# Performance work log

Hardware: AMD Instinct MI355X
Metric: run time of the kernel (lower is better)

The kernel has to match this reference:

```python
import jax, jax.numpy as jnp
import numpy as np
import math

D_MODEL = 1024
NUM_HEADS = 16
D_K = D_MODEL // NUM_HEADS
MAX_LEN = 2048
BATCH = 2
SEQ = 2048


def setup_inputs() -> dict:
    key = jax.random.key(0)
    ks = jax.random.split(key, 12)
    w_scale = 0.02  # realistic init scale for linear weights
    inp = {
        "q": jax.random.normal(ks[0], (BATCH, SEQ, D_MODEL), jnp.float32),
        "k": jax.random.normal(ks[1], (BATCH, SEQ, D_MODEL), jnp.float32),
        "v": jax.random.normal(ks[2], (BATCH, SEQ, D_MODEL), jnp.float32),
        # learned params
        "rel_emb": jax.random.normal(ks[3], (2 * MAX_LEN, D_K), jnp.float32),
        "wq": jax.random.normal(ks[4], (D_MODEL, D_MODEL), jnp.float32) * w_scale,
        "bq": jnp.zeros((D_MODEL,), jnp.float32),
        "wk": jax.random.normal(ks[5], (D_MODEL, D_MODEL), jnp.float32) * w_scale,
        "bk": jnp.zeros((D_MODEL,), jnp.float32),
        "wv": jax.random.normal(ks[6], (D_MODEL, D_MODEL), jnp.float32) * w_scale,
        "bv": jnp.zeros((D_MODEL,), jnp.float32),
        "wo": jax.random.normal(ks[7], (D_MODEL, D_MODEL), jnp.float32) * w_scale,
        "bo": jnp.zeros((D_MODEL,), jnp.float32),
    }
    return inp


def reference(q, k, v, rel_emb, wq, bq, wk, bk, wv, bv, wo, bo):
    B, L, D = q.shape
    H, dk = NUM_HEADS, D // NUM_HEADS

    def split_heads(x):  # [B, L, D] -> [B, H, L, dk]
        return x.reshape(B, L, H, dk).transpose(0, 2, 1, 3)

    qh = split_heads(q @ wq.T + bq)
    kh = split_heads(k @ wk.T + bk)
    vh = split_heads(v @ wv.T + bv)

    # relative positions: rel_pos[i, j] = (j - i) + MAX_LEN, in [0, 2*MAX_LEN)
    r = jnp.arange(L)
    rel_pos = r[None, :] - r[:, None] + MAX_LEN  # [L, L] int32

    content_score = jnp.einsum("bhid,bhjd->bhij", qh, kh)
    # pos_score[b,h,i,j] = q[b,h,i,:] . rel_emb[rel_pos[i,j], :]
    rel = rel_emb[rel_pos]  # [L, L, dk]
    pos_score = jnp.einsum("bhid,ijd->bhij", qh, rel)

    scores = (content_score + pos_score) / math.sqrt(dk)
    attn = jax.nn.softmax(scores, axis=-1)
    out = jnp.einsum("bhij,bhjd->bhid", attn, vh)  # [B, H, L, dk]
    out = out.transpose(0, 2, 1, 3).reshape(B, L, D)
    return out @ wo.T + bo
```

## Files before the change

### kernel.cpp

```cpp
#include <hip/hip_runtime.h>
#include <hip/hip_fp16.h>


typedef _Float16 f16;
typedef _Float16 f16x4 __attribute__((ext_vector_type(4)));
typedef _Float16 f16x8 __attribute__((ext_vector_type(8)));
typedef float    f32x4 __attribute__((ext_vector_type(4)));

#define NBATCH 2
#define NHEADS 16
#define DKDIM  64
#define SEQL   2048
#define DMODEL 1024
#define NTOK   4096
#define MAXLEN 2048

__global__ void cvt_f32_f16(const float* __restrict__ src, f16* __restrict__ dst, int n4) {
    int i = blockIdx.x * blockDim.x + threadIdx.x;
    if (i < n4) {
        float4 v = ((const float4*)src)[i];
        f16x4 h = { (f16)v.x, (f16)v.y, (f16)v.z, (f16)v.w };
        ((f16x4*)dst)[i] = h;
    }
}

__global__ __launch_bounds__(256) void qkv_proj(
    const float* __restrict__ qg, const float* __restrict__ kg, const float* __restrict__ vg,
    const float* __restrict__ wq, const float* __restrict__ wk, const float* __restrict__ wv,
    const float* __restrict__ bq, const float* __restrict__ bk, const float* __restrict__ bv,
    f16* __restrict__ qh, f16* __restrict__ kh, f16* __restrict__ vt)
{
    const int which = blockIdx.z;
    const float* X    = which == 0 ? qg : (which == 1 ? kg : vg);
    const float* W    = which == 0 ? wq : (which == 1 ? wk : wv);
    const float* bias = which == 0 ? bq : (which == 1 ? bk : bv);

    __shared__ f16 As[128][40];
    __shared__ f16 Bs[128][40];

    const int tid = threadIdx.x;
    const int lane = tid & 63;
    const int w = tid >> 6;
    const int wr = w >> 1, wc = w & 1;
    const int row0 = blockIdx.y * 128;
    const int col0 = blockIdx.x * 128;

    f32x4 acc[4][4] = {};

    for (int kk = 0; kk < DMODEL; kk += 32) {
        #pragma unroll
        for (int rep = 0; rep < 4; ++rep) {
            int idx = rep * 256 + tid;
            int r = idx >> 3, seg = idx & 7;
            float4 va = *(const float4*)&X[(size_t)(row0 + r) * DMODEL + kk + seg * 4];
            f16x4 ha = { (f16)va.x, (f16)va.y, (f16)va.z, (f16)va.w };
            *(f16x4*)&As[r][seg * 4] = ha;
            float4 vb = *(const float4*)&W[(size_t)(col0 + r) * DMODEL + kk + seg * 4];
            f16x4 hb = { (f16)vb.x, (f16)vb.y, (f16)vb.z, (f16)vb.w };
            *(f16x4*)&Bs[r][seg * 4] = hb;
        }
        __syncthreads();

        f16x8 a[4], b[4];
        #pragma unroll
        for (int mi = 0; mi < 4; ++mi)
            a[mi] = *(const f16x8*)&As[wr * 64 + mi * 16 + (lane & 15)][(lane >> 4) * 8];
        #pragma unroll
        for (int ni = 0; ni < 4; ++ni)
            b[ni] = *(const f16x8*)&Bs[wc * 64 + ni * 16 + (lane & 15)][(lane >> 4) * 8];
        #pragma unroll
        for (int mi = 0; mi < 4; ++mi)
            #pragma unroll
            for (int ni = 0; ni < 4; ++ni)
                acc[mi][ni] = __builtin_amdgcn_mfma_f32_16x16x32_f16(a[mi], b[ni], acc[mi][ni], 0, 0, 0);
        __syncthreads();
    }

    #pragma unroll
    for (int mi = 0; mi < 4; ++mi) {
        #pragma unroll
        for (int ni = 0; ni < 4; ++ni) {
            int col = col0 + wc * 64 + ni * 16 + (lane & 15);
            int h = col >> 6, d = col & 63;
            float bc = bias[col];
            #pragma unroll
            for (int r = 0; r < 4; ++r) {
                int row = row0 + wr * 64 + mi * 16 + (lane >> 4) * 4 + r;
                int b_ = row >> 11, l = row & 2047;
                float val = acc[mi][ni][r] + bc;
                if (which == 0)
                    qh[((size_t)((b_ * 16 + h) * 2048 + l)) * 64 + d] = (f16)val;
                else if (which == 1)
                    kh[((size_t)((b_ * 16 + h) * 2048 + l)) * 64 + d] = (f16)val;
                else
                    vt[((size_t)((b_ * 16 + h) * 64 + d)) * 2048 + l] = (f16)val;
            }
        }
    }
}

__global__ __launch_bounds__(256) void flash_attn(
    const f16* __restrict__ qh, const f16* __restrict__ kh, const f16* __restrict__ vt,
    const f16* __restrict__ rel, f16* __restrict__ att)
{
    const int tid = threadIdx.x, lane = tid & 63, w = tid >> 6;
    const int bh = blockIdx.y;
    const int b = bh >> 4, h = bh & 15;
    const int i0 = blockIdx.x * 64;

    __shared__ f16 Ks[64][72];
    __shared__ f16 Vs[64][72];
    __shared__ f16 Rb[128][72];
    __shared__ f16 Qr[64][128];
    __shared__ f16 Ps[4][16][72];

    const size_t base_kq = (size_t)bh * SEQL * DKDIM;

    #pragma unroll
    for (int rep = 0; rep < 2; ++rep) {
        int idx = rep * 256 + tid;
        int r = idx >> 3, c8 = idx & 7;
        *(int4*)&Qr[r][c8 * 8] = *(const int4*)&qh[base_kq + (size_t)(i0 + r) * 64 + c8 * 8];
    }
    __syncthreads();
    f16x8 aq[2];
    aq[0] = *(const f16x8*)&Qr[w * 16 + (lane & 15)][(lane >> 4) * 8];
    aq[1] = *(const f16x8*)&Qr[w * 16 + (lane & 15)][32 + (lane >> 4) * 8];
    __syncthreads();

    float mrun[4], lrun[4];
    f32x4 oacc[4] = {};
    #pragma unroll
    for (int r = 0; r < 4; ++r) { mrun[r] = -1e30f; lrun[r] = 0.f; }

    for (int j0 = 0; j0 < SEQL; j0 += 64) {
        #pragma unroll
        for (int rep = 0; rep < 2; ++rep) {
            int idx = rep * 256 + tid;
            int r = idx >> 3, c8 = idx & 7;
            *(int4*)&Ks[r][c8 * 8] = *(const int4*)&kh[base_kq + (size_t)(j0 + r) * 64 + c8 * 8];
            *(int4*)&Vs[r][c8 * 8] = *(const int4*)&vt[base_kq + (size_t)r * 2048 + j0 + c8 * 8];
        }
        const int p0 = j0 - i0 - 63 + MAXLEN;
        #pragma unroll
        for (int rep = 0; rep < 4; ++rep) {
            int idx = rep * 256 + tid;
            int r = idx >> 3, c8 = idx & 7;
            int p = p0 + r; if (p > 4095) p = 4095;
            *(int4*)&Rb[r][c8 * 8] = *(const int4*)&rel[(size_t)p * 64 + c8 * 8];
        }
        __syncthreads();

        f32x4 sacc[4] = {};
        #pragma unroll
        for (int nf = 0; nf < 4; ++nf)
            #pragma unroll
            for (int ks = 0; ks < 2; ++ks) {
                f16x8 bk = *(const f16x8*)&Ks[nf * 16 + (lane & 15)][ks * 32 + (lane >> 4) * 8];
                sacc[nf] = __builtin_amdgcn_mfma_f32_16x16x32_f16(aq[ks], bk, sacc[nf], 0, 0, 0);
            }
        f32x4 qracc[8] = {};
        #pragma unroll
        for (int pf = 0; pf < 8; ++pf)
            #pragma unroll
            for (int ks = 0; ks < 2; ++ks) {
                f16x8 br = *(const f16x8*)&Rb[pf * 16 + (lane & 15)][ks * 32 + (lane >> 4) * 8];
                qracc[pf] = __builtin_amdgcn_mfma_f32_16x16x32_f16(aq[ks], br, qracc[pf], 0, 0, 0);
            }
        #pragma unroll
        for (int pf = 0; pf < 8; ++pf)
            #pragma unroll
            for (int r = 0; r < 4; ++r)
                Qr[w * 16 + (lane >> 4) * 4 + r][pf * 16 + (lane & 15)] = (f16)qracc[pf][r];
        __syncthreads();

        float p_[4][4];
        #pragma unroll
        for (int nf = 0; nf < 4; ++nf)
            #pragma unroll
            for (int r = 0; r < 4; ++r) {
                int gi = w * 16 + (lane >> 4) * 4 + r;
                int jl = nf * 16 + (lane & 15);
                p_[nf][r] = (sacc[nf][r] + (float)Qr[gi][jl - gi + 63]) * 0.125f;
            }
        float scale[4];
        #pragma unroll
        for (int r = 0; r < 4; ++r) {
            float mx = fmaxf(fmaxf(p_[0][r], p_[1][r]), fmaxf(p_[2][r], p_[3][r]));
            #pragma unroll
            for (int m = 8; m >= 1; m >>= 1) mx = fmaxf(mx, __shfl_xor(mx, m, 64));
            float mnew = fmaxf(mrun[r], mx);
            scale[r] = __expf(mrun[r] - mnew);
            float sm = 0.f;
            #pragma unroll
            for (int nf = 0; nf < 4; ++nf) { p_[nf][r] = __expf(p_[nf][r] - mnew); sm += p_[nf][r]; }
            #pragma unroll
            for (int m = 8; m >= 1; m >>= 1) sm += __shfl_xor(sm, m, 64);
            lrun[r] = lrun[r] * scale[r] + sm;
            mrun[r] = mnew;
        }
        #pragma unroll
        for (int df = 0; df < 4; ++df)
            #pragma unroll
            for (int r = 0; r < 4; ++r) oacc[df][r] *= scale[r];

        #pragma unroll
        for (int nf = 0; nf < 4; ++nf)
            #pragma unroll
            for (int r = 0; r < 4; ++r)
                Ps[w][(lane >> 4) * 4 + r][nf * 16 + (lane & 15)] = (f16)p_[nf][r];
        __syncthreads();
        f16x8 pa[2];
        pa[0] = *(const f16x8*)&Ps[w][lane & 15][(lane >> 4) * 8];
        pa[1] = *(const f16x8*)&Ps[w][lane & 15][32 + (lane >> 4) * 8];
        #pragma unroll
        for (int df = 0; df < 4; ++df)
            #pragma unroll
            for (int ks = 0; ks < 2; ++ks) {
                f16x8 bv = *(const f16x8*)&Vs[df * 16 + (lane & 15)][ks * 32 + (lane >> 4) * 8];
                oacc[df] = __builtin_amdgcn_mfma_f32_16x16x32_f16(pa[ks], bv, oacc[df], 0, 0, 0);
            }
        __syncthreads();
    }

    #pragma unroll
    for (int df = 0; df < 4; ++df) {
        int d = df * 16 + (lane & 15);
        #pragma unroll
        for (int r = 0; r < 4; ++r) {
            int i = i0 + w * 16 + (lane >> 4) * 4 + r;
            float val = oacc[df][r] / lrun[r];
            att[((size_t)(b * 2048 + i)) * DMODEL + h * 64 + d] = (f16)val;
        }
    }
}

__global__ __launch_bounds__(256) void out_proj(
    const f16* __restrict__ att, const f16* __restrict__ wo16, const float* __restrict__ bo,
    float* __restrict__ out)
{
    __shared__ f16 As[128][40];
    __shared__ f16 Bs[128][40];
    const int tid = threadIdx.x, lane = tid & 63, w = tid >> 6;
    const int wr = w >> 1, wc = w & 1;
    const int row0 = blockIdx.y * 128, col0 = blockIdx.x * 128;

    f32x4 acc[4][4] = {};

    for (int kk = 0; kk < DMODEL; kk += 32) {
        #pragma unroll
        for (int rep = 0; rep < 2; ++rep) {
            int idx = rep * 256 + tid;
            int r = idx >> 2, c8 = idx & 3;
            *(int4*)&As[r][c8 * 8] = *(const int4*)&att[(size_t)(row0 + r) * DMODEL + kk + c8 * 8];
            *(int4*)&Bs[r][c8 * 8] = *(const int4*)&wo16[(size_t)(col0 + r) * DMODEL + kk + c8 * 8];
        }
        __syncthreads();

        f16x8 a[4], b[4];
        #pragma unroll
        for (int mi = 0; mi < 4; ++mi)
            a[mi] = *(const f16x8*)&As[wr * 64 + mi * 16 + (lane & 15)][(lane >> 4) * 8];
        #pragma unroll
        for (int ni = 0; ni < 4; ++ni)
            b[ni] = *(const f16x8*)&Bs[wc * 64 + ni * 16 + (lane & 15)][(lane >> 4) * 8];
        #pragma unroll
        for (int mi = 0; mi < 4; ++mi)
            #pragma unroll
            for (int ni = 0; ni < 4; ++ni)
                acc[mi][ni] = __builtin_amdgcn_mfma_f32_16x16x32_f16(a[mi], b[ni], acc[mi][ni], 0, 0, 0);
        __syncthreads();
    }

    #pragma unroll
    for (int mi = 0; mi < 4; ++mi)
        #pragma unroll
        for (int ni = 0; ni < 4; ++ni) {
            int col = col0 + wc * 64 + ni * 16 + (lane & 15);
            float bc = bo[col];
            #pragma unroll
            for (int r = 0; r < 4; ++r) {
                int row = row0 + wr * 64 + mi * 16 + (lane >> 4) * 4 + r;
                out[(size_t)row * DMODEL + col] = acc[mi][ni][r] + bc;
            }
        }
}

extern "C" void kernel_launch(void* const* d_in, const int* in_sizes, int n_in,
                              void* d_out, int out_size, void* d_ws, size_t ws_size,
                              hipStream_t stream) {
    const float* q   = (const float*)d_in[0];
    const float* k   = (const float*)d_in[1];
    const float* v   = (const float*)d_in[2];
    const float* rel = (const float*)d_in[3];
    const float* wq  = (const float*)d_in[4];
    const float* bq  = (const float*)d_in[5];
    const float* wk  = (const float*)d_in[6];
    const float* bk  = (const float*)d_in[7];
    const float* wv  = (const float*)d_in[8];
    const float* bv  = (const float*)d_in[9];
    const float* wo  = (const float*)d_in[10];
    const float* bo  = (const float*)d_in[11];
    float* out = (float*)d_out;

    f16* ws    = (f16*)d_ws;
    f16* wo16  = ws;
    f16* rel16 = wo16 + (size_t)DMODEL * DMODEL;
    f16* qh16  = rel16 + (size_t)2 * MAXLEN * DKDIM;
    f16* kh16  = qh16 + (size_t)NTOK * DMODEL;
    f16* vt16  = kh16 + (size_t)NTOK * DMODEL;
    f16* att16 = vt16 + (size_t)NTOK * DMODEL;

    cvt_f32_f16<<<dim3(1024), 256, 0, stream>>>(wo, wo16, DMODEL * DMODEL / 4);
    cvt_f32_f16<<<dim3(256),  256, 0, stream>>>(rel, rel16, 2 * MAXLEN * DKDIM / 4);
    qkv_proj<<<dim3(8, 32, 3), 256, 0, stream>>>(q, k, v, wq, wk, wv, bq, bk, bv,
                                                 qh16, kh16, vt16);
    flash_attn<<<dim3(32, 32), 256, 0, stream>>>(qh16, kh16, vt16, rel16, att16);
    out_proj<<<dim3(8, 32), 256, 0, stream>>>(att16, wo16, bo, out);
}
```

Baseline: 438.7 us.

## Ring-buffer rel embeddings, per-wave pos band, deeper GEMM K tiles

After: 394.4 us. 1.11x faster.

```diff
diff --git a/kernel.cpp b/kernel.cpp
--- a/kernel.cpp
+++ b/kernel.cpp
@@ -35,8 +35,8 @@
     const float* W    = which == 0 ? wq : (which == 1 ? wk : wv);
     const float* bias = which == 0 ? bq : (which == 1 ? bk : bv);
 
-    __shared__ f16 As[128][40];
-    __shared__ f16 Bs[128][40];
+    __shared__ f16 As[128][72];
+    __shared__ f16 Bs[128][72];
 
     const int tid = threadIdx.x;
     const int lane = tid & 63;
@@ -47,11 +47,11 @@
 
     f32x4 acc[4][4] = {};
 
-    for (int kk = 0; kk < DMODEL; kk += 32) {
-        #pragma unroll
-        for (int rep = 0; rep < 4; ++rep) {
+    for (int kk = 0; kk < DMODEL; kk += 64) {
+        #pragma unroll
+        for (int rep = 0; rep < 8; ++rep) {
             int idx = rep * 256 + tid;
-            int r = idx >> 3, seg = idx & 7;
+            int r = idx >> 4, seg = idx & 15;
             float4 va = *(const float4*)&X[(size_t)(row0 + r) * DMODEL + kk + seg * 4];
             f16x4 ha = { (f16)va.x, (f16)va.y, (f16)va.z, (f16)va.w };
             *(f16x4*)&As[r][seg * 4] = ha;
@@ -61,18 +61,26 @@
         }
         __syncthreads();
 
-        f16x8 a[4], b[4];
+        f16x8 a[4][2], b[4][2];
         #pragma unroll
         for (int mi = 0; mi < 4; ++mi)
-            a[mi] = *(const f16x8*)&As[wr * 64 + mi * 16 + (lane & 15)][(lane >> 4) * 8];
+            #pragma unroll
+            for (int ks = 0; ks < 2; ++ks)
+                a[mi][ks] = *(const f16x8*)&As[wr * 64 + mi * 16 + (lane & 15)][ks * 32 + (lane >> 4) * 8];
         #pragma unroll
         for (int ni = 0; ni < 4; ++ni)
-            b[ni] = *(const f16x8*)&Bs[wc * 64 + ni * 16 + (lane & 15)][(lane >> 4) * 8];
+            #pragma unroll
+            for (int ks = 0; ks < 2; ++ks)
+                b[ni][ks] = *(const f16x8*)&Bs[wc * 64 + ni * 16 + (lane & 15)][ks * 32 + (lane >> 4) * 8];
+        __builtin_amdgcn_s_setprio(1);
         #pragma unroll
         for (int mi = 0; mi < 4; ++mi)
             #pragma unroll
             for (int ni = 0; ni < 4; ++ni)
-                acc[mi][ni] = __builtin_amdgcn_mfma_f32_16x16x32_f16(a[mi], b[ni], acc[mi][ni], 0, 0, 0);
+                #pragma unroll
+                for (int ks = 0; ks < 2; ++ks)
+                    acc[mi][ni] = __builtin_amdgcn_mfma_f32_16x16x32_f16(a[mi][ks], b[ni][ks], acc[mi][ni], 0, 0, 0);
+        __builtin_amdgcn_s_setprio(0);
         __syncthreads();
     }
 
@@ -99,7 +107,7 @@
     }
 }
 
-__global__ __launch_bounds__(256) void flash_attn(
+__global__ __launch_bounds__(256, 3) void flash_attn(
     const f16* __restrict__ qh, const f16* __restrict__ kh, const f16* __restrict__ vt,
     const f16* __restrict__ rel, f16* __restrict__ att)
 {
@@ -111,21 +119,23 @@
     __shared__ f16 Ks[64][72];
     __shared__ f16 Vs[64][72];
     __shared__ f16 Rb[128][72];
-    __shared__ f16 Qr[64][128];
-    __shared__ f16 Ps[4][16][72];
+    __shared__ f16 Qb[4][16][88];
 
     const size_t base_kq = (size_t)bh * SEQL * DKDIM;
+    const int pb0 = MAXLEN - i0 - 63;
 
     #pragma unroll
     for (int rep = 0; rep < 2; ++rep) {
         int idx = rep * 256 + tid;
-        int r = idx >> 3, c8 = idx & 7;
-        *(int4*)&Qr[r][c8 * 8] = *(const int4*)&qh[base_kq + (size_t)(i0 + r) * 64 + c8 * 8];
+        int r = idx >> 3, seg = idx & 7;
+        *(int4*)&Ks[r][seg * 8] = *(const int4*)&qh[base_kq + (size_t)(i0 + r) * 64 + seg * 8];
+        int p = pb0 + r;
+        *(int4*)&Rb[p & 127][seg * 8] = *(const int4*)&rel[(size_t)p * 64 + seg * 8];
     }
     __syncthreads();
     f16x8 aq[2];
-    aq[0] = *(const f16x8*)&Qr[w * 16 + (lane & 15)][(lane >> 4) * 8];
-    aq[1] = *(const f16x8*)&Qr[w * 16 + (lane & 15)][32 + (lane >> 4) * 8];
+    aq[0] = *(const f16x8*)&Ks[w * 16 + (lane & 15)][(lane >> 4) * 8];
+    aq[1] = *(const f16x8*)&Ks[w * 16 + (lane & 15)][32 + (lane >> 4) * 8];
     __syncthreads();
 
     float mrun[4], lrun[4];
@@ -133,25 +143,26 @@
     #pragma unroll
     for (int r = 0; r < 4; ++r) { mrun[r] = -1e30f; lrun[r] = 0.f; }
 
+    const int p0w_off = 48 - w * 16;
+
     for (int j0 = 0; j0 < SEQL; j0 += 64) {
         #pragma unroll
         for (int rep = 0; rep < 2; ++rep) {
             int idx = rep * 256 + tid;
-            int r = idx >> 3, c8 = idx & 7;
-            *(int4*)&Ks[r][c8 * 8] = *(const int4*)&kh[base_kq + (size_t)(j0 + r) * 64 + c8 * 8];
-            *(int4*)&Vs[r][c8 * 8] = *(const int4*)&vt[base_kq + (size_t)r * 2048 + j0 + c8 * 8];
-        }
-        const int p0 = j0 - i0 - 63 + MAXLEN;
-        #pragma unroll
-        for (int rep = 0; rep < 4; ++rep) {
-            int idx = rep * 256 + tid;
-            int r = idx >> 3, c8 = idx & 7;
-            int p = p0 + r; if (p > 4095) p = 4095;
-            *(int4*)&Rb[r][c8 * 8] = *(const int4*)&rel[(size_t)p * 64 + c8 * 8];
-        }
-        __syncthreads();
-
+            int r = idx >> 3, seg = idx & 7;
+            *(int4*)&Ks[r][seg * 8] = *(const int4*)&kh[base_kq + (size_t)(j0 + r) * 64 + seg * 8];
+            *(int4*)&Vs[r][seg * 8] = *(const int4*)&vt[base_kq + (size_t)r * 2048 + j0 + seg * 8];
+            int p = pb0 + j0 + 64 + r;
+            int slot = p & 127;
+            if (p > 4095) p = 4095;
+            *(int4*)&Rb[slot][seg * 8] = *(const int4*)&rel[(size_t)p * 64 + seg * 8];
+        }
+        __syncthreads();
+
+        const int p0w = pb0 + j0 + p0w_off;
         f32x4 sacc[4] = {};
+        f32x4 qracc[5] = {};
+        __builtin_amdgcn_s_setprio(1);
         #pragma unroll
         for (int nf = 0; nf < 4; ++nf)
             #pragma unroll
@@ -159,29 +170,29 @@
                 f16x8 bk = *(const f16x8*)&Ks[nf * 16 + (lane & 15)][ks * 32 + (lane >> 4) * 8];
                 sacc[nf] = __builtin_amdgcn_mfma_f32_16x16x32_f16(aq[ks], bk, sacc[nf], 0, 0, 0);
             }
-        f32x4 qracc[8] = {};
-        #pragma unroll
-        for (int pf = 0; pf < 8; ++pf)
+        #pragma unroll
+        for (int pf = 0; pf < 5; ++pf)
             #pragma unroll
             for (int ks = 0; ks < 2; ++ks) {
-                f16x8 br = *(const f16x8*)&Rb[pf * 16 + (lane & 15)][ks * 32 + (lane >> 4) * 8];
+                f16x8 br = *(const f16x8*)&Rb[(p0w + pf * 16 + (lane & 15)) & 127][ks * 32 + (lane >> 4) * 8];
                 qracc[pf] = __builtin_amdgcn_mfma_f32_16x16x32_f16(aq[ks], br, qracc[pf], 0, 0, 0);
             }
-        #pragma unroll
-        for (int pf = 0; pf < 8; ++pf)
+        __builtin_amdgcn_s_setprio(0);
+
+        #pragma unroll
+        for (int pf = 0; pf < 5; ++pf)
             #pragma unroll
             for (int r = 0; r < 4; ++r)
-                Qr[w * 16 + (lane >> 4) * 4 + r][pf * 16 + (lane & 15)] = (f16)qracc[pf][r];
-        __syncthreads();
+                Qb[w][(lane >> 4) * 4 + r][pf * 16 + (lane & 15)] = (f16)qracc[pf][r];
 
         float p_[4][4];
         #pragma unroll
         for (int nf = 0; nf < 4; ++nf)
             #pragma unroll
             for (int r = 0; r < 4; ++r) {
-                int gi = w * 16 + (lane >> 4) * 4 + r;
-                int jl = nf * 16 + (lane & 15);
-                p_[nf][r] = (sacc[nf][r] + (float)Qr[gi][jl - gi + 63]) * 0.125f;
+                int gi = (lane >> 4) * 4 + r;
+                int c = nf * 16 + (lane & 15) - gi + 15;
+                p_[nf][r] = (sacc[nf][r] + (float)Qb[w][gi][c]) * 0.125f;
             }
         float scale[4];
         #pragma unroll
@@ -208,11 +219,11 @@
         for (int nf = 0; nf < 4; ++nf)
             #pragma unroll
             for (int r = 0; r < 4; ++r)
-                Ps[w][(lane >> 4) * 4 + r][nf * 16 + (lane & 15)] = (f16)p_[nf][r];
-        __syncthreads();
+                Qb[w][(lane >> 4) * 4 + r][nf * 16 + (lane & 15)] = (f16)p_[nf][r];
         f16x8 pa[2];
-        pa[0] = *(const f16x8*)&Ps[w][lane & 15][(lane >> 4) * 8];
-        pa[1] = *(const f16x8*)&Ps[w][lane & 15][32 + (lane >> 4) * 8];
+        pa[0] = *(const f16x8*)&Qb[w][lane & 15][(lane >> 4) * 8];
+        pa[1] = *(const f16x8*)&Qb[w][lane & 15][32 + (lane >> 4) * 8];
+        __builtin_amdgcn_s_setprio(1);
         #pragma unroll
         for (int df = 0; df < 4; ++df)
             #pragma unroll
@@ -220,6 +231,7 @@
                 f16x8 bv = *(const f16x8*)&Vs[df * 16 + (lane & 15)][ks * 32 + (lane >> 4) * 8];
                 oacc[df] = __builtin_amdgcn_mfma_f32_16x16x32_f16(pa[ks], bv, oacc[df], 0, 0, 0);
             }
+        __builtin_amdgcn_s_setprio(0);
         __syncthreads();
     }
 
@@ -239,36 +251,44 @@
     const f16* __restrict__ att, const f16* __restrict__ wo16, const float* __restrict__ bo,
     float* __restrict__ out)
 {
-    __shared__ f16 As[128][40];
-    __shared__ f16 Bs[128][40];
+    __shared__ f16 As[128][72];
+    __shared__ f16 Bs[128][72];
     const int tid = threadIdx.x, lane = tid & 63, w = tid >> 6;
     const int wr = w >> 1, wc = w & 1;
     const int row0 = blockIdx.y * 128, col0 = blockIdx.x * 128;
 
     f32x4 acc[4][4] = {};
 
-    for (int kk = 0; kk < DMODEL; kk += 32) {
-        #pragma unroll
-        for (int rep = 0; rep < 2; ++rep) {
+    for (int kk = 0; kk < DMODEL; kk += 64) {
+        #pragma unroll
+        for (int rep = 0; rep < 4; ++rep) {
             int idx = rep * 256 + tid;
-            int r = idx >> 2, c8 = idx & 3;
-            *(int4*)&As[r][c8 * 8] = *(const int4*)&att[(size_t)(row0 + r) * DMODEL + kk + c8 * 8];
-            *(int4*)&Bs[r][c8 * 8] = *(const int4*)&wo16[(size_t)(col0 + r) * DMODEL + kk + c8 * 8];
-        }
-        __syncthreads();
-
-        f16x8 a[4], b[4];
+            int r = idx >> 3, seg = idx & 7;
+            *(int4*)&As[r][seg * 8] = *(const int4*)&att[(size_t)(row0 + r) * DMODEL + kk + seg * 8];
+            *(int4*)&Bs[r][seg * 8] = *(const int4*)&wo16[(size_t)(col0 + r) * DMODEL + kk + seg * 8];
+        }
+        __syncthreads();
+
+        f16x8 a[4][2], b[4][2];
         #pragma unroll
         for (int mi = 0; mi < 4; ++mi)
-            a[mi] = *(const f16x8*)&As[wr * 64 + mi * 16 + (lane & 15)][(lane >> 4) * 8];
+            #pragma unroll
+            for (int ks = 0; ks < 2; ++ks)
+                a[mi][ks] = *(const f16x8*)&As[wr * 64 + mi * 16 + (lane & 15)][ks * 32 + (lane >> 4) * 8];
         #pragma unroll
         for (int ni = 0; ni < 4; ++ni)
-            b[ni] = *(const f16x8*)&Bs[wc * 64 + ni * 16 + (lane & 15)][(lane >> 4) * 8];
+            #pragma unroll
+            for (int ks = 0; ks < 2; ++ks)
+                b[ni][ks] = *(const f16x8*)&Bs[wc * 64 + ni * 16 + (lane & 15)][ks * 32 + (lane >> 4) * 8];
+        __builtin_amdgcn_s_setprio(1);
         #pragma unroll
         for (int mi = 0; mi < 4; ++mi)
             #pragma unroll
             for (int ni = 0; ni < 4; ++ni)
-                acc[mi][ni] = __builtin_amdgcn_mfma_f32_16x16x32_f16(a[mi], b[ni], acc[mi][ni], 0, 0, 0);
+                #pragma unroll
+                for (int ks = 0; ks < 2; ++ks)
+                    acc[mi][ni] = __builtin_amdgcn_mfma_f32_16x16x32_f16(a[mi][ks], b[ni][ks], acc[mi][ni], 0, 0, 0);
+        __builtin_amdgcn_s_setprio(0);
         __syncthreads();
     }
 
```
